# Kernel optimization log

Measured on AMD Instinct MI355X. Metric: run time of the kernel, lower is better.

The kernel has to match this reference:

```python
import jax, jax.numpy as jnp
import numpy as np

ACTION = np.array([1, 64, 128, 256, 512, 1024, 2048])
FIELD_DIMS = np.array([1000000, 500000, 250000, 100000, 100000, 50000, 50000, 10000, 10000,
                       5000, 5000, 1000, 1000, 500, 500, 200, 200, 100, 100, 50, 50, 20, 20, 10, 10, 4])
OFFSETS = np.concatenate([[0], np.cumsum(FIELD_DIMS)])[:-1].astype(np.int32)
TOTAL_VOCAB = int(FIELD_DIMS.sum())  # 2083764
F = len(FIELD_DIMS)  # 26 fields
A = len(ACTION)      # 7 candidate quantization sizes
DIM = 16
BATCH = 4096
TEMPERATURE = 1.0


def _prior_flag():
    # reproduces the masking logic from __init__
    flag = np.full((F, A), -100000.0, dtype=np.float32)
    for i in range(F):
        if FIELD_DIMS[i] < 150:
            flag[i, 0] = 1.0
        for k in range(1, A):
            if ACTION[k] * 2.5 > FIELD_DIMS[i]:
                break
            flag[i, k] = 1.0
    return flag

PRIOR_FLAG = _prior_flag()


def setup_inputs() -> dict:
    key = jax.random.key(0)
    ks = jax.random.split(key, 8)
    x = jax.random.randint(ks[0], (BATCH, F), 0, jnp.asarray(FIELD_DIMS)[None, :], dtype=jnp.int32)
    emb_table = jax.random.normal(ks[1], (TOTAL_VOCAB, DIM), dtype=jnp.float32) * 0.01
    lin_w = jax.random.normal(ks[2], (TOTAL_VOCAB, 1), dtype=jnp.float32) * 0.01
    lin_bias = jnp.zeros((1,), dtype=jnp.float32)
    codebooks = jax.random.normal(ks[3], (A - 1, F, int(ACTION[-1]), DIM), dtype=jnp.float32) * 0.01
    # per-action code assignments for every global feature id, values < ACTION[k]
    assignments = jax.random.randint(ks[4], (A - 1, TOTAL_VOCAB), 0,
                                     jnp.asarray(ACTION[1:])[:, None], dtype=jnp.int32)
    arch_params = jnp.full((F, A), 0.5, dtype=jnp.float32) + 0.001 * jax.random.normal(ks[5], (F, A))
    u = jax.random.uniform(ks[6], (F, A), minval=1e-6, maxval=1.0 - 1e-6)
    gumbel = -jnp.log(-jnp.log(u))
    return {"x": x, "emb_table": emb_table, "lin_w": lin_w, "lin_bias": lin_bias,
            "codebooks": codebooks, "assignments": assignments,
            "arch_params": arch_params, "gumbel": gumbel}


def reference(x, emb_table, lin_w, lin_bias, codebooks, assignments, arch_params, gumbel):
    prior = jnp.asarray(PRIOR_FLAG)
    # gumbel-softmax architecture weights per field over ACTION candidates
    logits = jnp.where(prior > 0, arch_params, -1e9)
    probs = jax.nn.softmax((logits + gumbel) / TEMPERATURE, axis=1)  # [F, A]

    gid = x + jnp.asarray(OFFSETS)[None, :]          # [B, F] global feature ids
    full = emb_table[gid]                            # [B, F, D] candidate 0 (no quantization)
    codes = assignments[:, gid]                      # [A-1, B, F]
    cand = codebooks[jnp.arange(A - 1)[:, None, None],
                     jnp.arange(F)[None, None, :], codes]  # [A-1, B, F, D]
    allc = jnp.concatenate([full[None], cand], axis=0)     # [A, B, F, D]
    x_emb = jnp.einsum('fa,abfd->bfd', probs, allc)        # weighted expert mix

    # FactorizationMachine(reduce_sum=True): 0.5 * (sum^2 - sum of squares)
    s = jnp.sum(x_emb, axis=1)                             # [B, D]
    fm = 0.5 * jnp.sum(s * s - jnp.sum(x_emb * x_emb, axis=1), axis=-1)  # [B]

    lin = jnp.sum(lin_w[gid][..., 0], axis=1) + lin_bias[0]             # [B]
    return lin + fm
```

## Files before the change

### kernel.cpp

```cpp
#include <hip/hip_runtime.h>

#define F 26
#define FPAD 32
#define A 7
#define DIM 16
#define BATCH 4096
#define TV 2083764

__device__ __constant__ int c_OFFSETS[F] = {
    0, 1000000, 1500000, 1750000, 1850000, 1950000, 2000000, 2050000,
    2060000, 2070000, 2075000, 2080000, 2081000, 2082000, 2082500, 2083000,
    2083200, 2083400, 2083500, 2083600, 2083650, 2083700, 2083720, 2083740,
    2083750, 2083760};
__device__ __constant__ int c_FIELD_DIMS[F] = {
    1000000, 500000, 250000, 100000, 100000, 50000, 50000, 10000, 10000,
    5000, 5000, 1000, 1000, 500, 500, 200, 200, 100, 100, 50, 50, 20, 20,
    10, 10, 4};
__device__ __constant__ int c_ACTION[A] = {1, 64, 128, 256, 512, 1024, 2048};

__global__ __launch_bounds__(256, 4) void gsq_fm_kernel(
    const int* __restrict__ x,
    const float* __restrict__ emb_table,
    const float* __restrict__ lin_w,
    const float* __restrict__ lin_bias,
    const float* __restrict__ codebooks,
    const int* __restrict__ assignments,
    const float* __restrict__ arch,
    const float* __restrict__ gumbel,
    float* __restrict__ out)
{
    __shared__ float probs_s[FPAD][A];
    __shared__ int gid_s[4][FPAD];

    const int t = threadIdx.x;

    if (t < 128) {
        const int e = t >> 5;
        const int fi = t & 31;
        gid_s[e][fi] = (fi < F)
            ? (x[(blockIdx.x * 4 + e) * F + fi] + c_OFFSETS[fi])
            : 0;
    }

    if (t >= 128 && t < 128 + FPAD) {
        const int f = t - 128;
        if (f < F) {
            const int dims = c_FIELD_DIMS[f];
            float z[A];
            float m = -1e30f;
            for (int k = 0; k < A; ++k) {
                bool allowed = (k == 0) ? (dims < 150)
                                        : (5 * c_ACTION[k] <= 2 * dims);
                float logit = allowed ? arch[f * A + k] : -1e9f;
                z[k] = logit + gumbel[f * A + k];
                m = fmaxf(m, z[k]);
            }
            float ssum = 0.f;
            for (int k = 0; k < A; ++k) {
                z[k] = expf(z[k] - m);
                ssum += z[k];
            }
            const float inv = 1.f / ssum;
            for (int k = 0; k < A; ++k) probs_s[f][k] = z[k] * inv;
        } else {
            for (int k = 0; k < A; ++k) probs_s[f][k] = 0.f;
        }
    }
    __syncthreads();

    const int lane = t & 63;
    const int e = t >> 6;
    const int b = blockIdx.x * 4 + e;
    const int sub = lane >> 2;
    const int dh = lane & 3;

    float sx = 0.f, sy = 0.f, sz = 0.f, sw = 0.f;
    float q = 0.f;
    float lin = 0.f;

#pragma unroll
    for (int j = 0; j < 2; ++j) {
        const int f = sub + 16 * j;
        const int gid = gid_s[e][f];
        const bool valid = (f < F);

        const float p0 = probs_s[f][0];
        const int eoff = (p0 != 0.f) ? gid * DIM : 0;
        const float4 er = *(const float4*)&emb_table[eoff + 4 * dh];
        float xx = p0 * er.x, xy = p0 * er.y, xz = p0 * er.z, xw = p0 * er.w;

        float wgt[6];
        int coff[6];
#pragma unroll
        for (int a = 0; a < 6; ++a) {
            wgt[a] = probs_s[f][a + 1];
            const bool live = (wgt[a] != 0.f);
            const int aaddr = live ? (a * TV + gid) : 0;
            const int code = assignments[aaddr];
            coff[a] = live ? (((a * F + f) * 2048 + code) * DIM) : 0;
        }
#pragma unroll
        for (int a = 0; a < 6; ++a) {
            const float4 r = *(const float4*)&codebooks[coff[a] + 4 * dh];
            xx = fmaf(wgt[a], r.x, xx);
            xy = fmaf(wgt[a], r.y, xy);
            xz = fmaf(wgt[a], r.z, xz);
            xw = fmaf(wgt[a], r.w, xw);
        }

        sx += xx; sy += xy; sz += xz; sw += xw;
        q = fmaf(xx, xx, q);
        q = fmaf(xy, xy, q);
        q = fmaf(xz, xz, q);
        q = fmaf(xw, xw, q);

        const float lm = (dh == 0 && valid) ? 1.f : 0.f;
        const float lv = lin_w[valid ? gid : 0];
        lin = fmaf(lm, lv, lin);
    }

    sx += __shfl_xor(sx, 4, 64);  sx += __shfl_xor(sx, 8, 64);
    sx += __shfl_xor(sx, 16, 64); sx += __shfl_xor(sx, 32, 64);
    sy += __shfl_xor(sy, 4, 64);  sy += __shfl_xor(sy, 8, 64);
    sy += __shfl_xor(sy, 16, 64); sy += __shfl_xor(sy, 32, 64);
    sz += __shfl_xor(sz, 4, 64);  sz += __shfl_xor(sz, 8, 64);
    sz += __shfl_xor(sz, 16, 64); sz += __shfl_xor(sz, 32, 64);
    sw += __shfl_xor(sw, 4, 64);  sw += __shfl_xor(sw, 8, 64);
    sw += __shfl_xor(sw, 16, 64); sw += __shfl_xor(sw, 32, 64);

    q += __shfl_xor(q, 1, 64);  q += __shfl_xor(q, 2, 64);
    q += __shfl_xor(q, 4, 64);  q += __shfl_xor(q, 8, 64);
    q += __shfl_xor(q, 16, 64); q += __shfl_xor(q, 32, 64);
    lin += __shfl_xor(lin, 1, 64);  lin += __shfl_xor(lin, 2, 64);
    lin += __shfl_xor(lin, 4, 64);  lin += __shfl_xor(lin, 8, 64);
    lin += __shfl_xor(lin, 16, 64); lin += __shfl_xor(lin, 32, 64);

    float val = sx * sx + sy * sy + sz * sz + sw * sw;
    val += __shfl_xor(val, 1, 64);
    val += __shfl_xor(val, 2, 64);

    if (lane == 0) {
        out[b] = lin + lin_bias[0] + 0.5f * (val - q);
    }
}

extern "C" void kernel_launch(void* const* d_in, const int* in_sizes, int n_in,
                              void* d_out, int out_size, void* d_ws, size_t ws_size,
                              hipStream_t stream) {
    const int*   x           = (const int*)d_in[0];
    const float* emb_table   = (const float*)d_in[1];
    const float* lin_w       = (const float*)d_in[2];
    const float* lin_bias    = (const float*)d_in[3];
    const float* codebooks   = (const float*)d_in[4];
    const int*   assignments = (const int*)d_in[5];
    const float* arch        = (const float*)d_in[6];
    const float* gumbel      = (const float*)d_in[7];
    float* out = (float*)d_out;

    dim3 grid(BATCH / 4);
    dim3 block(256);
    hipLaunchKernelGGL(gsq_fm_kernel, grid, block, 0, stream,
                       x, emb_table, lin_w, lin_bias, codebooks, assignments,
                       arch, gumbel, out);
}
```

Measured before the change: 14.43 us.

## Split field loop across two wavefronts per sample with shared-memory reduction

Each batch sample is now handled by two wavefronts, one per half of the fields, instead of one wavefront looping over both halves. Partial sums, squares and linear terms are combined through shared memory after an extra block barrier. The grid doubles to BATCH/2 blocks and the launch bound now asks for 8 blocks per CU. The aim is more wavefronts in flight to hide gather latency, paid for with an extra __syncthreads, shared-memory traffic, and duplicate per-block setup work such as the softmax.

After: 13.65 us (median of 2 runs). -5.4%, faster.

```diff
diff --git a/kernel.cpp b/kernel.cpp
--- a/kernel.cpp
+++ b/kernel.cpp
@@ -18,7 +18,7 @@
     10, 10, 4};
 __device__ __constant__ int c_ACTION[A] = {1, 64, 128, 256, 512, 1024, 2048};
 
-__global__ __launch_bounds__(256, 4) void gsq_fm_kernel(
+__global__ __launch_bounds__(256, 8) void gsq_fm_kernel(
     const int* __restrict__ x,
     const float* __restrict__ emb_table,
     const float* __restrict__ lin_w,
@@ -30,20 +30,23 @@
     float* __restrict__ out)
 {
     __shared__ float probs_s[FPAD][A];
-    __shared__ int gid_s[4][FPAD];
+    __shared__ int gid_s[2][FPAD];
+    __shared__ float4 s_red[2][2][4];
+    __shared__ float q_red[2][2];
+    __shared__ float lin_red[2][2];
 
     const int t = threadIdx.x;
 
-    if (t < 128) {
+    if (t < 64) {
         const int e = t >> 5;
         const int fi = t & 31;
         gid_s[e][fi] = (fi < F)
-            ? (x[(blockIdx.x * 4 + e) * F + fi] + c_OFFSETS[fi])
+            ? (x[(blockIdx.x * 2 + e) * F + fi] + c_OFFSETS[fi])
             : 0;
     }
 
-    if (t >= 128 && t < 128 + FPAD) {
-        const int f = t - 128;
+    if (t >= 64 && t < 64 + FPAD) {
+        const int f = t - 64;
         if (f < F) {
             const int dims = c_FIELD_DIMS[f];
             float z[A];
@@ -69,56 +72,47 @@
     __syncthreads();
 
     const int lane = t & 63;
-    const int e = t >> 6;
-    const int b = blockIdx.x * 4 + e;
+    const int h = (t >> 6) & 1;
+    const int e = t >> 7;
+    const int b = blockIdx.x * 2 + e;
     const int sub = lane >> 2;
     const int dh = lane & 3;
 
-    float sx = 0.f, sy = 0.f, sz = 0.f, sw = 0.f;
-    float q = 0.f;
-    float lin = 0.f;
+    const int f = h * 16 + sub;
+    const int gid = gid_s[e][f];
+    const bool valid = (f < F);
 
+    const float p0 = probs_s[f][0];
+    const int eoff = (p0 != 0.f) ? gid * DIM : 0;
+    const float4 er = *(const float4*)&emb_table[eoff + 4 * dh];
+    float xx = p0 * er.x, xy = p0 * er.y, xz = p0 * er.z, xw = p0 * er.w;
+
+    float wgt[6];
+    int coff[6];
 #pragma unroll
-    for (int j = 0; j < 2; ++j) {
-        const int f = sub + 16 * j;
-        const int gid = gid_s[e][f];
-        const bool valid = (f < F);
-
-        const float p0 = probs_s[f][0];
-        const int eoff = (p0 != 0.f) ? gid * DIM : 0;
-        const float4 er = *(const float4*)&emb_table[eoff + 4 * dh];
-        float xx = p0 * er.x, xy = p0 * er.y, xz = p0 * er.z, xw = p0 * er.w;
-
-        float wgt[6];
-        int coff[6];
+    for (int a = 0; a < 6; ++a) {
+        wgt[a] = probs_s[f][a + 1];
+        const bool live = (wgt[a] != 0.f);
+        const int aaddr = live ? (a * TV + gid) : 0;
+        const int code = assignments[aaddr];
+        coff[a] = live ? (((a * F + f) * 2048 + code) * DIM) : 0;
+    }
 #pragma unroll
-        for (int a = 0; a < 6; ++a) {
-            wgt[a] = probs_s[f][a + 1];
-            const bool live = (wgt[a] != 0.f);
-            const int aaddr = live ? (a * TV + gid) : 0;
-            const int code = assignments[aaddr];
-            coff[a] = live ? (((a * F + f) * 2048 + code) * DIM) : 0;
-        }
-#pragma unroll
-        for (int a = 0; a < 6; ++a) {
-            const float4 r = *(const float4*)&codebooks[coff[a] + 4 * dh];
-            xx = fmaf(wgt[a], r.x, xx);
-            xy = fmaf(wgt[a], r.y, xy);
-            xz = fmaf(wgt[a], r.z, xz);
-            xw = fmaf(wgt[a], r.w, xw);
-        }
-
-        sx += xx; sy += xy; sz += xz; sw += xw;
-        q = fmaf(xx, xx, q);
-        q = fmaf(xy, xy, q);
-        q = fmaf(xz, xz, q);
-        q = fmaf(xw, xw, q);
-
-        const float lm = (dh == 0 && valid) ? 1.f : 0.f;
-        const float lv = lin_w[valid ? gid : 0];
-        lin = fmaf(lm, lv, lin);
+    for (int a = 0; a < 6; ++a) {
+        const float4 r = *(const float4*)&codebooks[coff[a] + 4 * dh];
+        xx = fmaf(wgt[a], r.x, xx);
+        xy = fmaf(wgt[a], r.y, xy);
+        xz = fmaf(wgt[a], r.z, xz);
+        xw = fmaf(wgt[a], r.w, xw);
     }
 
+    float q = xx * xx + xy * xy + xz * xz + xw * xw;
+
+    const float lm = (dh == 0 && valid) ? 1.f : 0.f;
+    const float lv = lin_w[valid ? gid : 0];
+    float lin = lm * lv;
+
+    float sx = xx, sy = xy, sz = xz, sw = xw;
     sx += __shfl_xor(sx, 4, 64);  sx += __shfl_xor(sx, 8, 64);
     sx += __shfl_xor(sx, 16, 64); sx += __shfl_xor(sx, 32, 64);
     sy += __shfl_xor(sy, 4, 64);  sy += __shfl_xor(sy, 8, 64);
@@ -135,12 +129,28 @@
     lin += __shfl_xor(lin, 4, 64);  lin += __shfl_xor(lin, 8, 64);
     lin += __shfl_xor(lin, 16, 64); lin += __shfl_xor(lin, 32, 64);
 
-    float val = sx * sx + sy * sy + sz * sz + sw * sw;
-    val += __shfl_xor(val, 1, 64);
-    val += __shfl_xor(val, 2, 64);
+    if (lane < 4) {
+        s_red[e][h][lane] = make_float4(sx, sy, sz, sw);
+    }
+    if (lane == 0) {
+        q_red[e][h] = q;
+        lin_red[e][h] = lin;
+    }
+    __syncthreads();
 
-    if (lane == 0) {
-        out[b] = lin + lin_bias[0] + 0.5f * (val - q);
+    if (h == 0) {
+        const float4 a0 = s_red[e][0][dh];
+        const float4 a1 = s_red[e][1][dh];
+        const float tx = a0.x + a1.x, ty = a0.y + a1.y;
+        const float tz = a0.z + a1.z, tw = a0.w + a1.w;
+        float val = tx * tx + ty * ty + tz * tz + tw * tw;
+        val += __shfl_xor(val, 1, 64);
+        val += __shfl_xor(val, 2, 64);
+        if (lane == 0) {
+            const float qt = q_red[e][0] + q_red[e][1];
+            const float lt = lin_red[e][0] + lin_red[e][1];
+            out[b] = lt + lin_bias[0] + 0.5f * (val - qt);
+        }
     }
 }
 
@@ -157,7 +167,7 @@
     const float* gumbel      = (const float*)d_in[7];
     float* out = (float*)d_out;
 
-    dim3 grid(BATCH / 4);
+    dim3 grid(BATCH / 2);
     dim3 block(256);
     hipLaunchKernelGGL(gsq_fm_kernel, grid, block, 0, stream,
                        x, emb_table, lin_w, lin_bias, codebooks, assignments,
```
